# Kernel optimization log

Measured on AMD Instinct MI355X. Metric: run time of the kernel, lower is better.

Reference implementation:

```python
import jax, jax.numpy as jnp
import numpy as np

N_NODES = 100000
N_EDGES = 1600000
N_GRAPHS = 64
D_IN, D_HID, D_OUT = 128, 256, 128


def gcn_conv(x, src, dst, W, b, n_nodes):
    """PyG-style GCNConv: x @ W, add self-loops, sym-normalize, scatter-add src->dst, + bias."""
    h = x @ W  # (N, out)
    loop = jnp.arange(n_nodes, dtype=src.dtype)
    src_f = jnp.concatenate([src, loop])
    dst_f = jnp.concatenate([dst, loop])
    deg = jax.ops.segment_sum(jnp.ones_like(dst_f, dtype=h.dtype), dst_f, num_segments=n_nodes)
    dinv = jnp.where(deg > 0, jax.lax.rsqrt(deg), 0.0)
    norm = dinv[src_f] * dinv[dst_f]  # (E+N,)
    msg = h[src_f] * norm[:, None]    # (E+N, out)  -- dominant memory traffic
    out = jax.ops.segment_sum(msg, dst_f, num_segments=n_nodes)
    return out + b


def setup_inputs() -> dict:
    key = jax.random.key(0)
    k1, k2, k3, k4, k5 = jax.random.split(key, 5)
    x = jax.random.normal(k1, (N_NODES, D_IN), dtype=jnp.float32)
    edge_index = jax.random.randint(k2, (2, N_EDGES), 0, N_NODES, dtype=jnp.int64)
    batch = jnp.sort(jax.random.randint(k3, (N_NODES,), 0, N_GRAPHS, dtype=jnp.int64))
    W1 = jax.random.normal(k4, (D_IN, D_HID), dtype=jnp.float32) * (1.0 / np.sqrt(D_IN))
    b1 = jnp.zeros((D_HID,), dtype=jnp.float32)
    W2 = jax.random.normal(k5, (D_HID, D_OUT), dtype=jnp.float32) * (1.0 / np.sqrt(D_HID))
    b2 = jnpps = jnp.zeros((D_OUT,), dtype=jnp.float32)
    return {"x": x, "edge_index": edge_index, "batch": batch,
            "W1": W1, "b1": b1, "W2": W2, "b2": b2}


def reference(x, edge_index, batch, W1, b1, W2, b2):
    src, dst = edge_index[0], edge_index[1]
    n = x.shape[0]
    h = gcn_conv(x, src, dst, W1, b1, n)
    h = jax.nn.relu(h)
    h = gcn_conv(h, src, dst, W2, b2, n)
    # global_add_pool
    return jax.ops.segment_sum(h, batch, num_segments=N_GRAPHS)
```

## Files before the change

kernel.cpp:

```cpp
#include <hip/hip_runtime.h>

#define NN 100000
#define NNPAD 100352
#define NE 1600000
#define NG 64
#define DI 128
#define DH 256
#define DO 128
#define SEG2 25088
#define NPART 256
#define PSTRIDE 392
#define PCAP 7168

using short8 = __attribute__((ext_vector_type(8))) short;
using f32x4  = __attribute__((ext_vector_type(4))) float;

__device__ __forceinline__ float bf2f(unsigned short u) {
    return __uint_as_float(((unsigned)u) << 16);
}
__device__ __forceinline__ unsigned short f2bf(float f) {
    unsigned u = __float_as_uint(f);
    unsigned r = (u + 0x7FFFu + ((u >> 16) & 1u)) >> 16;
    return (unsigned short)r;
}

__global__ void k_prep(const float* __restrict__ x, unsigned short* __restrict__ xbf,
                       const float* __restrict__ W1, unsigned short* __restrict__ w1t,
                       int* __restrict__ pcur) {
    int i = blockIdx.x * blockDim.x + threadIdx.x;
    const int NX4 = NN * 32;
    if (i < NX4) {
        float4 v = ((const float4*)x)[i];
        ushort4 o;
        o.x = f2bf(v.x); o.y = f2bf(v.y); o.z = f2bf(v.z); o.w = f2bf(v.w);
        ((ushort4*)xbf)[i] = o;
    } else if (i < NX4 + DI * DH) {
        int t = i - NX4;
        int k = t / DH, n = t % DH;
        w1t[n * DI + k] = f2bf(W1[t]);
    }
    if (i < NPART) pcur[i] = i * PCAP;
}

__global__ __launch_bounds__(256) void k_partition(const int* __restrict__ src,
        const int* __restrict__ dst, int* __restrict__ pcur,
        int2* __restrict__ pe, int e) {
    __shared__ int hist[NPART];
    __shared__ int curb[NPART];
    const int EPT = 16;
    int t = threadIdx.x;
    hist[t] = 0;
    __syncthreads();
    int base = blockIdx.x * (256 * EPT) + t;
    int sA[EPT], dA[EPT];
#pragma unroll
    for (int k = 0; k < EPT; ++k) {
        int i = base + k * 256;
        if (i < e) {
            sA[k] = src[i]; dA[k] = dst[i];
            atomicAdd(&hist[dA[k] / PSTRIDE], 1);
        } else dA[k] = -1;
    }
    __syncthreads();
    curb[t] = atomicAdd(&pcur[t], hist[t]);
    __syncthreads();
#pragma unroll
    for (int k = 0; k < EPT; ++k) {
        if (dA[k] >= 0) {
            int b = dA[k] / PSTRIDE;
            int pos = atomicAdd(&curb[b], 1);
            pe[pos] = make_int2(sA[k], dA[k]);
        }
    }
}

__global__ __launch_bounds__(256) void k_count(const int2* __restrict__ pe,
        const int* __restrict__ pcur, int* __restrict__ cnt) {
    __shared__ int c[PSTRIDE];
    int p = blockIdx.x;
    int lo = p * PSTRIDE;
    int t = threadIdx.x;
    for (int i = t; i < PSTRIDE; i += 256) c[i] = 0;
    __syncthreads();
    int j1 = pcur[p];
    for (int j = p * PCAP + t; j < j1; j += 256)
        atomicAdd(&c[pe[j].y - lo], 1);
    __syncthreads();
    for (int i = t; i < PSTRIDE; i += 256) {
        int d = lo + i;
        if (d < NN) cnt[d] = c[i];
    }
}


__global__ void k_scan1(const int* __restrict__ in, int* __restrict__ out,
                        int* __restrict__ bsum, int n) {
    __shared__ int sh[256];
    int t = threadIdx.x;
    int i = blockIdx.x * 256 + t;
    int v = (i < n) ? in[i] : 0;
    sh[t] = v;
    __syncthreads();
    for (int off = 1; off < 256; off <<= 1) {
        int add = (t >= off) ? sh[t - off] : 0;
        __syncthreads();
        sh[t] += add;
        __syncthreads();
    }
    if (i < n) out[i] = sh[t] - v;
    if (t == 255) bsum[blockIdx.x] = sh[255];
}
__global__ void k_scan2(int* __restrict__ bsum, int* __restrict__ cntg, int nb) {
    __shared__ int sh[512];
    int t = threadIdx.x;
    if (t < NG) cntg[t] = 0;
    int v = (t < nb) ? bsum[t] : 0;
    sh[t] = v;
    __syncthreads();
    for (int off = 1; off < 512; off <<= 1) {
        int add = (t >= off) ? sh[t - off] : 0;
        __syncthreads();
        sh[t] += add;
        __syncthreads();
    }
    if (t < nb) bsum[t] = sh[t] - v;
}
__global__ void k_scan3(int* __restrict__ rowst, const int* __restrict__ bsum,
                        const int* __restrict__ deg, float* __restrict__ dinv,
                        const int* __restrict__ batch, int2* __restrict__ gdv,
                        int* __restrict__ cntg, int n, int total) {
    __shared__ int sh[NG];
    int t = threadIdx.x;
    if (t < NG) sh[t] = 0;
    __syncthreads();
    int i = blockIdx.x * 256 + t;
    if (i < n) {
        float dv = rsqrtf((float)(deg[i] + 1));
        dinv[i] = dv;
        int b = batch[i];
        int2 g; g.x = __float_as_int(dv); g.y = b;
        gdv[i] = g;
        atomicAdd(&sh[b], 1);
        rowst[i] += bsum[blockIdx.x];
    }
    if (i == 0) rowst[n] = total;
    __syncthreads();
    if (t < NG && sh[t]) atomicAdd(&cntg[t], sh[t]);
}

__global__ __launch_bounds__(256) void k_place(const int2* __restrict__ pe,
        const int* __restrict__ pcur, const int* __restrict__ rowst,
        const float* __restrict__ dinv, int2* __restrict__ csr8) {
    __shared__ int cur[PSTRIDE];
    __shared__ float dl[PSTRIDE];
    int p = blockIdx.x;
    int lo = p * PSTRIDE;
    int t = threadIdx.x;
    for (int i = t; i < PSTRIDE; i += 256) {
        int d = lo + i;
        cur[i] = (d < NN) ? rowst[d] : 0;
        dl[i]  = (d < NN) ? dinv[d] : 0.f;
    }
    __syncthreads();
    int j1 = pcur[p];
    for (int j = p * PCAP + t; j < j1; j += 256) {
        int2 ed = pe[j];
        int a = ed.y - lo;
        float w = dinv[ed.x] * dl[a];
        int pos = atomicAdd(&cur[a], 1);
        csr8[pos] = make_int2(ed.x, __float_as_int(w));
    }
}

__global__ __launch_bounds__(256) void k_cmbuild(const int2* __restrict__ csr8,
        const int* __restrict__ rowst, const int* __restrict__ batch,
        const int2* __restrict__ gdv, float* __restrict__ cmT) {
    __shared__ float acc[SEG2];
    int g   = blockIdx.x >> 2;
    int seg = blockIdx.x & 3;
    int slo = seg * SEG2;
    int t = threadIdx.x;
    for (int i = t; i < SEG2; i += 256) acc[i] = 0.f;

    int lo = 0, hi = NN;
    while (lo < hi) { int m = (lo + hi) >> 1; if (batch[m] < g) lo = m + 1; else hi = m; }
    int dstart = lo;
    int lo2 = lo, hi2 = NN;
    while (lo2 < hi2) { int m = (lo2 + hi2) >> 1; if (batch[m] < g + 1) lo2 = m + 1; else hi2 = m; }
    int e0 = rowst[dstart], e1 = rowst[lo2];
    __syncthreads();

    int j = e0 + t;
    for (; j + 768 < e1; j += 1024) {
        int2 p0 = csr8[j];
        int2 p1 = csr8[j + 256];
        int2 p2 = csr8[j + 512];
        int2 p3 = csr8[j + 768];
        int a0 = p0.x - slo, a1 = p1.x - slo, a2 = p2.x - slo, a3 = p3.x - slo;
        if ((unsigned)a0 < SEG2) atomicAdd(&acc[a0], __int_as_float(p0.y));
        if ((unsigned)a1 < SEG2) atomicAdd(&acc[a1], __int_as_float(p1.y));
        if ((unsigned)a2 < SEG2) atomicAdd(&acc[a2], __int_as_float(p2.y));
        if ((unsigned)a3 < SEG2) atomicAdd(&acc[a3], __int_as_float(p3.y));
    }
    for (; j < e1; j += 256) {
        int2 p = csr8[j];
        int a = p.x - slo;
        if ((unsigned)a < SEG2) atomicAdd(&acc[a], __int_as_float(p.y));
    }
    __syncthreads();

    float* row = cmT + (size_t)g * NNPAD;
    for (int i = t; i < SEG2; i += 256) {
        int s = slo + i;
        float v = acc[i];
        if (s < NN) {
            int2 gv = gdv[s];
            if (gv.y == g) { float dv = __int_as_float(gv.x); v += dv * dv; }
        }
        row[s] = v;
    }
}

__global__ __launch_bounds__(256) void k_agg16(const unsigned short* __restrict__ feat,
        const int2* __restrict__ csr8, const int* __restrict__ row_start,
        const float* __restrict__ dinv, unsigned short* __restrict__ out, int n) {
    int gid = blockIdx.x * blockDim.x + threadIdx.x;
    int node = gid >> 4;
    int lane = threadIdx.x & 15;
    if (node >= n) return;
    const short8* f8 = (const short8*)feat;
    float wd = dinv[node];
    float wd2 = wd * wd;
    short8 a = f8[(size_t)node * 16 + lane];
    float acc[8];
#pragma unroll
    for (int i = 0; i < 8; ++i) acc[i] = bf2f((unsigned short)a[i]) * wd2;
    int j = row_start[node], end = row_start[node + 1];
    for (; j + 3 < end; j += 4) {
        int2 p0 = csr8[j], p1 = csr8[j + 1], p2 = csr8[j + 2], p3 = csr8[j + 3];
        float w0 = __int_as_float(p0.y), w1 = __int_as_float(p1.y);
        float w2 = __int_as_float(p2.y), w3 = __int_as_float(p3.y);
        short8 v0 = f8[(size_t)p0.x * 16 + lane];
        short8 v1 = f8[(size_t)p1.x * 16 + lane];
        short8 v2 = f8[(size_t)p2.x * 16 + lane];
        short8 v3 = f8[(size_t)p3.x * 16 + lane];
#pragma unroll
        for (int i = 0; i < 8; ++i)
            acc[i] += w0 * bf2f((unsigned short)v0[i]) + w1 * bf2f((unsigned short)v1[i])
                    + w2 * bf2f((unsigned short)v2[i]) + w3 * bf2f((unsigned short)v3[i]);
    }
    for (; j < end; ++j) {
        int2 p = csr8[j];
        float w = __int_as_float(p.y);
        short8 v = f8[(size_t)p.x * 16 + lane];
#pragma unroll
        for (int i = 0; i < 8; ++i) acc[i] += w * bf2f((unsigned short)v[i]);
    }
    short8 o;
#pragma unroll
    for (int i = 0; i < 8; ++i) o[i] = (short)f2bf(acc[i]);
    ((short8*)out)[(size_t)node * 16 + lane] = o;
}

__global__ __launch_bounds__(512) void k_fused(const unsigned short* __restrict__ agg1,
        const unsigned short* __restrict__ w1t, const float* __restrict__ b1,
        const float* __restrict__ cmT, float* __restrict__ partial) {
    __shared__ unsigned short Ws[256 * 128];
    __shared__ unsigned short As[64 * 128];
    __shared__ unsigned short Hs[256 * 64];
    __shared__ unsigned short Cs[64 * 64];

    const int tid = threadIdx.x;
    const int sb = blockIdx.x * 512;

#pragma unroll
    for (int i = 0; i < 8; ++i) {
        int c = tid + i * 512;
        int row = c >> 4, seg = c & 15;
        uint4 v = *(const uint4*)(w1t + row * 128 + seg * 8);
        *(uint4*)((char*)Ws + row * 256 + ((seg * 16) ^ ((row & 7) << 4))) = v;
    }

    const int w  = tid >> 6;
    const int l  = tid & 63;
    const int lr = l & 15;
    const int lg = l >> 4;
    const int swz = (lr & 7) << 4;
    const int j0 = w * 32;

    float bb0 = b1[j0 + lr];
    float bb1 = b1[j0 + 16 + lr];

    f32x4 acc2[4][2] = {};

    for (int c = 0; c < 8; ++c) {
        int s0 = sb + c * 64;
        __syncthreads();
#pragma unroll
        for (int i = 0; i < 2; ++i) {
            int cc = tid + i * 512;
            int row = cc >> 4, seg = cc & 15;
            uint4 v = make_uint4(0, 0, 0, 0);
            int node = s0 + row;
            if (node < NN) v = *(const uint4*)(agg1 + (size_t)node * 128 + seg * 8);
            *(uint4*)((char*)As + row * 256 + ((seg * 16) ^ ((row & 7) << 4))) = v;
        }
        {
            int g = tid >> 3, seg = tid & 7;
            const float* cp = cmT + (size_t)g * NNPAD + s0 + seg * 8;
            float4 f0 = *(const float4*)cp;
            float4 f1 = *(const float4*)(cp + 4);
            uint4 v;
            v.x = (unsigned)f2bf(f0.x) | ((unsigned)f2bf(f0.y) << 16);
            v.y = (unsigned)f2bf(f0.z) | ((unsigned)f2bf(f0.w) << 16);
            v.z = (unsigned)f2bf(f1.x) | ((unsigned)f2bf(f1.y) << 16);
            v.w = (unsigned)f2bf(f1.z) | ((unsigned)f2bf(f1.w) << 16);
            *(uint4*)((char*)Cs + g * 128 + ((seg * 16) ^ ((g & 7) << 4))) = v;
        }
        __syncthreads();

        f32x4 accA[4][2] = {};
#pragma unroll
        for (int ks = 0; ks < 4; ++ks) {
            int kb = ks * 64 + lg * 16;
            short8 a[4];
#pragma unroll
            for (int m = 0; m < 4; ++m)
                a[m] = *(const short8*)((const char*)As + (m * 16 + lr) * 256 + (kb ^ swz));
#pragma unroll
            for (int n = 0; n < 2; ++n) {
                short8 b = *(const short8*)((const char*)Ws + (j0 + n * 16 + lr) * 256 + (kb ^ swz));
#pragma unroll
                for (int m = 0; m < 4; ++m)
                    accA[m][n] = __builtin_amdgcn_mfma_f32_16x16x32_bf16(a[m], b, accA[m][n], 0, 0, 0);
            }
        }
#pragma unroll
        for (int n = 0; n < 2; ++n) {
            int j = j0 + n * 16 + lr;
            float bbv = n ? bb1 : bb0;
#pragma unroll
            for (int m = 0; m < 4; ++m) {
                float v0 = fmaxf(accA[m][n][0] + bbv, 0.f);
                float v1 = fmaxf(accA[m][n][1] + bbv, 0.f);
                float v2 = fmaxf(accA[m][n][2] + bbv, 0.f);
                float v3 = fmaxf(accA[m][n][3] + bbv, 0.f);
                uint2 p;
                p.x = (unsigned)f2bf(v0) | ((unsigned)f2bf(v1) << 16);
                p.y = (unsigned)f2bf(v2) | ((unsigned)f2bf(v3) << 16);
                *(uint2*)((char*)Hs + j * 128 + (((m * 16 + lg * 4) * 2) ^ swz)) = p;
            }
        }
        __syncthreads();

#pragma unroll
        for (int ks = 0; ks < 2; ++ks) {
            int kb = ks * 64 + lg * 16;
            short8 a[4];
#pragma unroll
            for (int mg = 0; mg < 4; ++mg)
                a[mg] = *(const short8*)((const char*)Cs + (mg * 16 + lr) * 128 + (kb ^ swz));
#pragma unroll
            for (int n = 0; n < 2; ++n) {
                short8 b = *(const short8*)((const char*)Hs + (j0 + n * 16 + lr) * 128 + (kb ^ swz));
#pragma unroll
                for (int mg = 0; mg < 4; ++mg)
                    acc2[mg][n] = __builtin_amdgcn_mfma_f32_16x16x32_bf16(a[mg], b, acc2[mg][n], 0, 0, 0);
            }
        }
    }

    float* pb = partial + (size_t)blockIdx.x * (NG * DH);
#pragma unroll
    for (int mg = 0; mg < 4; ++mg)
#pragma unroll
        for (int n = 0; n < 2; ++n)
#pragma unroll
            for (int r = 0; r < 4; ++r) {
                int g = mg * 16 + lg * 4 + r;
                int j = j0 + n * 16 + lr;
                pb[g * DH + j] = acc2[mg][n][r];
            }
}

__global__ __launch_bounds__(256) void k_tail(const float* __restrict__ partial,
        const float* __restrict__ W2, const float* __restrict__ b2,
        const int* __restrict__ cntg, float* __restrict__ out) {
    __shared__ float pre[DH];
    int g = blockIdx.x;
    int t = threadIdx.x;
    float s0 = 0.f, s1 = 0.f, s2 = 0.f, s3 = 0.f;
    for (int b = 0; b < 196; b += 4) {
        s0 += partial[(size_t)b * (NG * DH) + g * DH + t];
        s1 += partial[(size_t)(b + 1) * (NG * DH) + g * DH + t];
        s2 += partial[(size_t)(b + 2) * (NG * DH) + g * DH + t];
        s3 += partial[(size_t)(b + 3) * (NG * DH) + g * DH + t];
    }
    pre[t] = (s0 + s1) + (s2 + s3);
    __syncthreads();
    if (t < DO) {
        float acc = (float)cntg[g] * b2[t];
        for (int k = 0; k < DH; ++k)
            acc = fmaf(pre[k], W2[k * DO + t], acc);
        out[g * DO + t] = acc;
    }
}


extern "C" void kernel_launch(void* const* d_in, const int* in_sizes, int n_in,
                              void* d_out, int out_size, void* d_ws, size_t ws_size,
                              hipStream_t stream) {
    const float* x     = (const float*)d_in[0];
    const int*   ei    = (const int*)d_in[1];
    const int*   batch = (const int*)d_in[2];
    const float* W1    = (const float*)d_in[3];
    const float* b1    = (const float*)d_in[4];
    const float* W2    = (const float*)d_in[5];
    const float* b2    = (const float*)d_in[6];
    float* out = (float*)d_out;

    const int* src = ei;
    const int* dst = ei + NE;

    char* ws = (char*)d_ws;
    float*          dinv    = (float*)(ws + 0);
    int*            cnt_in  = (int*)(ws + 524288);
    int*            rowst   = (int*)(ws + 1048576);
    int*            bsum    = (int*)(ws + 1572864);
    int*            cntg    = (int*)(ws + 1576960);
    unsigned short* w1t     = (unsigned short*)(ws + 1577216);
    int2*           gdv     = (int2*)(ws + 1642752);
    int2*           csr8    = (int2*)(ws + 2443264);
    unsigned short* xbf     = (unsigned short*)(ws + 15243264);
    unsigned short* agg1    = (unsigned short*)(ws + 40843264);
    float*          cmT     = (float*)(ws + 66443264);
    float*          partial = (float*)(ws + 92133376);
    int2*           pe      = (int2*)(ws + 104978432);
    int*            pcur    = (int*)(ws + 119658496);

    const int BLK = 256;
    auto cdiv = [](int a, int b) { return (a + b - 1) / b; };
    const int NB = cdiv(NN, 256);

    k_prep<<<cdiv(NN * 32 + DI * DH, BLK), BLK, 0, stream>>>(x, xbf, W1, w1t, pcur);

    k_partition<<<cdiv(NE, 256 * 16), 256, 0, stream>>>(src, dst, pcur, pe, NE);

    k_count<<<NPART, 256, 0, stream>>>(pe, pcur, cnt_in);

    k_scan1<<<NB, 256, 0, stream>>>(cnt_in, rowst, bsum, NN);
    k_scan2<<<1, 512, 0, stream>>>(bsum, cntg, NB);
    k_scan3<<<NB, 256, 0, stream>>>(rowst, bsum, cnt_in, dinv, batch, gdv, cntg, NN, NE);

    k_place<<<NPART, 256, 0, stream>>>(pe, pcur, rowst, dinv, csr8);

    k_cmbuild<<<NG * 4, 256, 0, stream>>>(csr8, rowst, batch, gdv, cmT);

    k_agg16<<<cdiv(NN * 16, BLK), BLK, 0, stream>>>(xbf, csr8, rowst, dinv, agg1, NN);

    k_fused<<<NNPAD / 512, 512, 0, stream>>>(agg1, w1t, b1, cmT, partial);

    k_tail<<<NG, 256, 0, stream>>>(partial, W2, b2, cntg, out);
}
```

Baseline: 230.8 us.

## Fuse edge partitioning into prep kernel and scan per partition in count

Merges the edge partition pass into the bf16 conversion kernel as extra blocks, with a memset replacing the in-kernel pcur init. The counts are now stored relative to each partition base. The count kernel also performs a local exclusive scan over each partition's nodes, so the separate first-level scan is dropped and a 256-entry partition-offset scan replaces it. The aggregation loop gains an 8-wide unrolled gather to put more loads in flight. Together these cut kernel launches and a pass over the degree array, at the cost of a larger mixed-role kernel and more register pressure in the aggregation.

Measured after the change: 229.3 us. About the same (-0.6%).

```diff
diff --git a/kernel.cpp b/kernel.cpp
--- a/kernel.cpp
+++ b/kernel.cpp
@@ -11,6 +11,7 @@
 #define NPART 256
 #define PSTRIDE 392
 #define PCAP 7168
+#define PB 391
 
 using short8 = __attribute__((ext_vector_type(8))) short;
 using f32x4  = __attribute__((ext_vector_type(4))) float;
@@ -24,10 +25,41 @@
     return (unsigned short)r;
 }
 
-__global__ void k_prep(const float* __restrict__ x, unsigned short* __restrict__ xbf,
-                       const float* __restrict__ W1, unsigned short* __restrict__ w1t,
-                       int* __restrict__ pcur) {
-    int i = blockIdx.x * blockDim.x + threadIdx.x;
+__global__ __launch_bounds__(256) void k_prep(const float* __restrict__ x,
+        unsigned short* __restrict__ xbf, const float* __restrict__ W1,
+        unsigned short* __restrict__ w1t, const int* __restrict__ src,
+        const int* __restrict__ dst, int* __restrict__ pcur, int2* __restrict__ pe) {
+    int t = threadIdx.x;
+    if (blockIdx.x < PB) {
+        __shared__ int hist[NPART];
+        __shared__ int curb[NPART];
+        const int EPT = 16;
+        hist[t] = 0;
+        __syncthreads();
+        int base = blockIdx.x * (256 * EPT) + t;
+        int sA[EPT], dA[EPT];
+#pragma unroll
+        for (int k = 0; k < EPT; ++k) {
+            int i = base + k * 256;
+            if (i < NE) {
+                sA[k] = src[i]; dA[k] = dst[i];
+                atomicAdd(&hist[dA[k] / PSTRIDE], 1);
+            } else dA[k] = -1;
+        }
+        __syncthreads();
+        curb[t] = t * PCAP + atomicAdd(&pcur[t], hist[t]);
+        __syncthreads();
+#pragma unroll
+        for (int k = 0; k < EPT; ++k) {
+            if (dA[k] >= 0) {
+                int b = dA[k] / PSTRIDE;
+                int pos = atomicAdd(&curb[b], 1);
+                pe[pos] = make_int2(sA[k], dA[k]);
+            }
+        }
+        return;
+    }
+    int i = (blockIdx.x - PB) * 256 + t;
     const int NX4 = NN * 32;
     if (i < NX4) {
         float4 v = ((const float4*)x)[i];
@@ -35,70 +67,49 @@
         o.x = f2bf(v.x); o.y = f2bf(v.y); o.z = f2bf(v.z); o.w = f2bf(v.w);
         ((ushort4*)xbf)[i] = o;
     } else if (i < NX4 + DI * DH) {
-        int t = i - NX4;
-        int k = t / DH, n = t % DH;
-        w1t[n * DI + k] = f2bf(W1[t]);
-    }
-    if (i < NPART) pcur[i] = i * PCAP;
-}
-
-__global__ __launch_bounds__(256) void k_partition(const int* __restrict__ src,
-        const int* __restrict__ dst, int* __restrict__ pcur,
-        int2* __restrict__ pe, int e) {
-    __shared__ int hist[NPART];
-    __shared__ int curb[NPART];
-    const int EPT = 16;
-    int t = threadIdx.x;
-    hist[t] = 0;
-    __syncthreads();
-    int base = blockIdx.x * (256 * EPT) + t;
-    int sA[EPT], dA[EPT];
-#pragma unroll
-    for (int k = 0; k < EPT; ++k) {
-        int i = base + k * 256;
-        if (i < e) {
-            sA[k] = src[i]; dA[k] = dst[i];
-            atomicAdd(&hist[dA[k] / PSTRIDE], 1);
-        } else dA[k] = -1;
-    }
-    __syncthreads();
-    curb[t] = atomicAdd(&pcur[t], hist[t]);
-    __syncthreads();
-#pragma unroll
-    for (int k = 0; k < EPT; ++k) {
-        if (dA[k] >= 0) {
-            int b = dA[k] / PSTRIDE;
-            int pos = atomicAdd(&curb[b], 1);
-            pe[pos] = make_int2(sA[k], dA[k]);
-        }
+        int tt = i - NX4;
+        int k = tt / DH, n = tt % DH;
+        w1t[n * DI + k] = f2bf(W1[tt]);
     }
 }
 
 __global__ __launch_bounds__(256) void k_count(const int2* __restrict__ pe,
-        const int* __restrict__ pcur, int* __restrict__ cnt) {
-    __shared__ int c[PSTRIDE];
+        const int* __restrict__ pcur, int* __restrict__ cnt,
+        int* __restrict__ rowst, int* __restrict__ pt) {
+    __shared__ int c[512];
     int p = blockIdx.x;
     int lo = p * PSTRIDE;
     int t = threadIdx.x;
-    for (int i = t; i < PSTRIDE; i += 256) c[i] = 0;
-    __syncthreads();
-    int j1 = pcur[p];
+    c[t] = 0; c[t + 256] = 0;
+    __syncthreads();
+    int j1 = p * PCAP + pcur[p];
     for (int j = p * PCAP + t; j < j1; j += 256)
         atomicAdd(&c[pe[j].y - lo], 1);
     __syncthreads();
-    for (int i = t; i < PSTRIDE; i += 256) {
-        int d = lo + i;
-        if (d < NN) cnt[d] = c[i];
-    }
-}
-
-
-__global__ void k_scan1(const int* __restrict__ in, int* __restrict__ out,
-                        int* __restrict__ bsum, int n) {
+    int cc0 = c[t], cc1 = c[t + 256];
+    for (int off = 1; off < 512; off <<= 1) {
+        int v0 = (t >= off) ? c[t - off] : 0;
+        int v1 = (t + 256 >= off) ? c[t + 256 - off] : 0;
+        __syncthreads();
+        c[t] += v0; c[t + 256] += v1;
+        __syncthreads();
+    }
+    if (t < PSTRIDE) {
+        int d = lo + t;
+        if (d < NN) { cnt[d] = cc0; rowst[d] = c[t] - cc0; }
+    }
+    if (t + 256 < PSTRIDE) {
+        int d = lo + t + 256;
+        if (d < NN) { cnt[d] = cc1; rowst[d] = c[t + 256] - cc1; }
+    }
+    if (t == 0) pt[p] = c[511];
+}
+
+__global__ void k_scan2p(int* __restrict__ pt, int* __restrict__ cntg) {
     __shared__ int sh[256];
     int t = threadIdx.x;
-    int i = blockIdx.x * 256 + t;
-    int v = (i < n) ? in[i] : 0;
+    if (t < NG) cntg[t] = 0;
+    int v = pt[t];
     sh[t] = v;
     __syncthreads();
     for (int off = 1; off < 256; off <<= 1) {
@@ -107,25 +118,10 @@
         sh[t] += add;
         __syncthreads();
     }
-    if (i < n) out[i] = sh[t] - v;
-    if (t == 255) bsum[blockIdx.x] = sh[255];
-}
-__global__ void k_scan2(int* __restrict__ bsum, int* __restrict__ cntg, int nb) {
-    __shared__ int sh[512];
-    int t = threadIdx.x;
-    if (t < NG) cntg[t] = 0;
-    int v = (t < nb) ? bsum[t] : 0;
-    sh[t] = v;
-    __syncthreads();
-    for (int off = 1; off < 512; off <<= 1) {
-        int add = (t >= off) ? sh[t - off] : 0;
-        __syncthreads();
-        sh[t] += add;
-        __syncthreads();
-    }
-    if (t < nb) bsum[t] = sh[t] - v;
-}
-__global__ void k_scan3(int* __restrict__ rowst, const int* __restrict__ bsum,
+    pt[t] = sh[t] - v;
+}
+
+__global__ void k_scan3(int* __restrict__ rowst, const int* __restrict__ pt,
                         const int* __restrict__ deg, float* __restrict__ dinv,
                         const int* __restrict__ batch, int2* __restrict__ gdv,
                         int* __restrict__ cntg, int n, int total) {
@@ -141,7 +137,7 @@
         int2 g; g.x = __float_as_int(dv); g.y = b;
         gdv[i] = g;
         atomicAdd(&sh[b], 1);
-        rowst[i] += bsum[blockIdx.x];
+        rowst[i] += pt[i / PSTRIDE];
     }
     if (i == 0) rowst[n] = total;
     __syncthreads();
@@ -162,7 +158,7 @@
         dl[i]  = (d < NN) ? dinv[d] : 0.f;
     }
     __syncthreads();
-    int j1 = pcur[p];
+    int j1 = p * PCAP + pcur[p];
     for (int j = p * PCAP + t; j < j1; j += 256) {
         int2 ed = pe[j];
         int a = ed.y - lo;
@@ -236,6 +232,28 @@
 #pragma unroll
     for (int i = 0; i < 8; ++i) acc[i] = bf2f((unsigned short)a[i]) * wd2;
     int j = row_start[node], end = row_start[node + 1];
+    for (; j + 7 < end; j += 8) {
+        int2 p0 = csr8[j],     p1 = csr8[j + 1], p2 = csr8[j + 2], p3 = csr8[j + 3];
+        int2 p4 = csr8[j + 4], p5 = csr8[j + 5], p6 = csr8[j + 6], p7 = csr8[j + 7];
+        short8 v0 = f8[(size_t)p0.x * 16 + lane];
+        short8 v1 = f8[(size_t)p1.x * 16 + lane];
+        short8 v2 = f8[(size_t)p2.x * 16 + lane];
+        short8 v3 = f8[(size_t)p3.x * 16 + lane];
+        short8 v4 = f8[(size_t)p4.x * 16 + lane];
+        short8 v5 = f8[(size_t)p5.x * 16 + lane];
+        short8 v6 = f8[(size_t)p6.x * 16 + lane];
+        short8 v7 = f8[(size_t)p7.x * 16 + lane];
+        float w0 = __int_as_float(p0.y), w1 = __int_as_float(p1.y);
+        float w2 = __int_as_float(p2.y), w3 = __int_as_float(p3.y);
+        float w4 = __int_as_float(p4.y), w5 = __int_as_float(p5.y);
+        float w6 = __int_as_float(p6.y), w7 = __int_as_float(p7.y);
+#pragma unroll
+        for (int i = 0; i < 8; ++i)
+            acc[i] += w0 * bf2f((unsigned short)v0[i]) + w1 * bf2f((unsigned short)v1[i])
+                    + w2 * bf2f((unsigned short)v2[i]) + w3 * bf2f((unsigned short)v3[i])
+                    + w4 * bf2f((unsigned short)v4[i]) + w5 * bf2f((unsigned short)v5[i])
+                    + w6 * bf2f((unsigned short)v6[i]) + w7 * bf2f((unsigned short)v7[i]);
+    }
     for (; j + 3 < end; j += 4) {
         int2 p0 = csr8[j], p1 = csr8[j + 1], p2 = csr8[j + 2], p3 = csr8[j + 3];
         float w0 = __int_as_float(p0.y), w1 = __int_as_float(p1.y);
@@ -426,7 +444,7 @@
     float*          dinv    = (float*)(ws + 0);
     int*            cnt_in  = (int*)(ws + 524288);
     int*            rowst   = (int*)(ws + 1048576);
-    int*            bsum    = (int*)(ws + 1572864);
+    int*            pt      = (int*)(ws + 1572864);
     int*            cntg    = (int*)(ws + 1576960);
     unsigned short* w1t     = (unsigned short*)(ws + 1577216);
     int2*           gdv     = (int2*)(ws + 1642752);
@@ -442,15 +460,17 @@
     auto cdiv = [](int a, int b) { return (a + b - 1) / b; };
     const int NB = cdiv(NN, 256);
 
-    k_prep<<<cdiv(NN * 32 + DI * DH, BLK), BLK, 0, stream>>>(x, xbf, W1, w1t, pcur);
-
-    k_partition<<<cdiv(NE, 256 * 16), 256, 0, stream>>>(src, dst, pcur, pe, NE);
-
-    k_count<<<NPART, 256, 0, stream>>>(pe, pcur, cnt_in);
-
-    k_scan1<<<NB, 256, 0, stream>>>(cnt_in, rowst, bsum, NN);
-    k_scan2<<<1, 512, 0, stream>>>(bsum, cntg, NB);
-    k_scan3<<<NB, 256, 0, stream>>>(rowst, bsum, cnt_in, dinv, batch, gdv, cntg, NN, NE);
+    hipMemsetAsync(pcur, 0, NPART * 4, stream);
+
+    {
+        int prep_blocks = cdiv(NN * 32 + DI * DH, BLK);
+        k_prep<<<PB + prep_blocks, BLK, 0, stream>>>(x, xbf, W1, w1t, src, dst, pcur, pe);
+    }
+
+    k_count<<<NPART, 256, 0, stream>>>(pe, pcur, cnt_in, rowst, pt);
+
+    k_scan2p<<<1, 256, 0, stream>>>(pt, cntg);
+    k_scan3<<<NB, 256, 0, stream>>>(rowst, pt, cnt_in, dinv, batch, gdv, cntg, NN, NE);
 
     k_place<<<NPART, 256, 0, stream>>>(pe, pcur, rowst, dinv, csr8);
 
```
